# Performance work log

Hardware: AMD Instinct MI355X
Metric: run time of the kernel (lower is better)

Reference implementation:

```python
import jax, jax.numpy as jnp
import numpy as np

B, D_MODEL, D_INNER, N_STATE, K = 128, 2048, 4096, 128, 4


def setup_inputs() -> dict:
    key = jax.random.key(0)
    ks = jax.random.split(key, 10)
    def n(k, shape, s=1.0):
        return jax.random.normal(k, shape, dtype=jnp.float32) * s
    return {
        "x_t": n(ks[0], (B, D_MODEL)),
        "conv_state": n(ks[1], (B, D_INNER, K - 1)),
        "ssm_state": n(ks[2], (B, N_STATE, D_INNER), 0.1),
        "W_in": n(ks[3], (2 * D_INNER, D_MODEL), 0.02),
        "b_in": jnp.zeros((2 * D_INNER,), jnp.float32),
        "conv_weight": n(ks[4], (D_INNER, K), 0.1),
        # A = -exp(A_log) is always negative; sample in (-1, 0) for stability
        "A": -jax.random.uniform(ks[5], (N_STATE, D_INNER), dtype=jnp.float32),
        "B_param": n(ks[6], (N_STATE,), 0.1),
        "C_param": n(ks[7], (N_STATE,), 0.1),
        "D_param": jnp.ones((D_INNER,), jnp.float32),
        "W_out": n(ks[8], (D_MODEL, D_INNER), 0.02),
        "b_out": jnp.zeros((D_MODEL,), jnp.float32),
    }


def reference(x_t, conv_state, ssm_state, W_in, b_in, conv_weight, A,
              B_param, C_param, D_param, W_out, b_out):
    # in_proj, keep first d_inner channels (as in forward())
    x_proj = (x_t @ W_in.T + b_in)[:, :D_INNER]                      # (B, Di)
    # rolling causal conv update: window = [old K-1 samples, new sample]
    window = jnp.concatenate([conv_state, x_proj[:, :, None]], axis=-1)  # (B, Di, K)
    u = jax.nn.silu(jnp.sum(window * conv_weight[None], axis=-1))    # (B, Di)
    new_conv_state = window[:, :, 1:]                                 # (B, Di, K-1)
    # discretized SSM recurrence: h' = exp(A)*h + B u ; y = C.h + D u
    dA = jnp.exp(A)                                                   # (N, Di), in (e^-1, 1)
    new_ssm_state = dA[None] * ssm_state + B_param[None, :, None] * u[:, None, :]  # (B, N, Di)
    y_inner = jnp.einsum('n,bnd->bd', C_param, new_ssm_state) + D_param * u         # (B, Di)
    # out_proj back to d_model
    y_t = y_inner @ W_out.T + b_out                                   # (B, D)
    return (y_t, new_conv_state, new_ssm_state)
```

## Files before the change

### kernel.cpp

```cpp
#include <hip/hip_runtime.h>
#include <hip/hip_bf16.h>

#define DI 4096
#define DM 2048
#define NS 128
#define BB 128

typedef __attribute__((ext_vector_type(8))) short bf16x8;
typedef __attribute__((ext_vector_type(4))) float f32x4;

__device__ __forceinline__ unsigned short f2bf(float f) {
  union { __hip_bfloat16 h; unsigned short u; } c;
  c.h = __float2bfloat16(f);
  return c.u;
}

template<int N, int K, int NSPLIT>
__global__ __launch_bounds__(256) void gemm_bf16(
    const float* __restrict__ Xg, const float* __restrict__ Wg,
    float* __restrict__ part) {
  constexpr int NBLKS = N / 32;
  constexpr int KS = K / NSPLIT;
  constexpr int NSTEPS = KS / 32;
  const int nblk = blockIdx.x % NBLKS;
  const int ks   = blockIdx.x / NBLKS;
  const int kbase = ks * KS;
  const int tid = threadIdx.x;
  const int lane = tid & 63;
  const int wid = tid >> 6;
  const int wr = wid & 1;
  const int wc = wid >> 1;
  const int r16 = lane & 15;
  const int kb = lane >> 4;

  __shared__ __hip_bfloat16 As[128][40];
  __shared__ __hip_bfloat16 Bs[32][40];

  const int arow = tid >> 3;
  const int seg  = tid & 7;

  f32x4 acc[4] = { {0,0,0,0}, {0,0,0,0}, {0,0,0,0}, {0,0,0,0} };

  const float* aG = Xg + (size_t)arow * K + kbase + seg * 4;
  const float* bG = Wg + (size_t)(nblk * 32 + arow) * K + kbase + seg * 4;

  float4 pa0 = *(const float4*)(aG + 0 * 32 * K);
  float4 pa1 = *(const float4*)(aG + 1 * 32 * K);
  float4 pa2 = *(const float4*)(aG + 2 * 32 * K);
  float4 pa3 = *(const float4*)(aG + 3 * 32 * K);
  float4 pb  = *(const float4*)(bG);

  for (int step = 0; step < NSTEPS; ++step) {
    if (step) __syncthreads();
    {
      ushort4 h;
      h.x = f2bf(pa0.x); h.y = f2bf(pa0.y); h.z = f2bf(pa0.z); h.w = f2bf(pa0.w);
      *(ushort4*)&As[arow +  0][seg * 4] = h;
      h.x = f2bf(pa1.x); h.y = f2bf(pa1.y); h.z = f2bf(pa1.z); h.w = f2bf(pa1.w);
      *(ushort4*)&As[arow + 32][seg * 4] = h;
      h.x = f2bf(pa2.x); h.y = f2bf(pa2.y); h.z = f2bf(pa2.z); h.w = f2bf(pa2.w);
      *(ushort4*)&As[arow + 64][seg * 4] = h;
      h.x = f2bf(pa3.x); h.y = f2bf(pa3.y); h.z = f2bf(pa3.z); h.w = f2bf(pa3.w);
      *(ushort4*)&As[arow + 96][seg * 4] = h;
      h.x = f2bf(pb.x);  h.y = f2bf(pb.y);  h.z = f2bf(pb.z);  h.w = f2bf(pb.w);
      *(ushort4*)&Bs[arow][seg * 4] = h;
    }
    if (step + 1 < NSTEPS) {
      const float* aN = aG + (step + 1) * 32;
      pa0 = *(const float4*)(aN + 0 * 32 * K);
      pa1 = *(const float4*)(aN + 1 * 32 * K);
      pa2 = *(const float4*)(aN + 2 * 32 * K);
      pa3 = *(const float4*)(aN + 3 * 32 * K);
      pb  = *(const float4*)(bG + (step + 1) * 32);
    }
    __syncthreads();
    bf16x8 bv = *(const bf16x8*)&Bs[wc * 16 + r16][kb * 8];
#pragma unroll
    for (int m = 0; m < 4; ++m) {
      bf16x8 av = *(const bf16x8*)&As[wr * 64 + m * 16 + r16][kb * 8];
      acc[m] = __builtin_amdgcn_mfma_f32_16x16x32_bf16(av, bv, acc[m], 0, 0, 0);
    }
  }

  const int ncol = nblk * 32 + wc * 16 + r16;
#pragma unroll
  for (int m = 0; m < 4; ++m) {
#pragma unroll
    for (int r = 0; r < 4; ++r) {
      int brow = wr * 64 + m * 16 + kb * 4 + r;
      part[(size_t)(ks * 128 + brow) * N + ncol] = acc[m][r];
    }
  }
}

__global__ __launch_bounds__(256) void combine1(
    const float* __restrict__ part, const float* __restrict__ b_in,
    const float* __restrict__ conv_state, const float* __restrict__ conv_weight,
    float* __restrict__ u_ws, float* __restrict__ ncs) {
  int idx = blockIdx.x * 256 + threadIdx.x;
  int d = idx & (DI - 1);
  float xp = b_in[d];
#pragma unroll
  for (int s = 0; s < 4; ++s) xp += part[(size_t)s * (BB * DI) + idx];
  const float* cs = conv_state + (size_t)idx * 3;
  float4 w4 = *(const float4*)(conv_weight + d * 4);
  float c0 = cs[0], c1 = cs[1], c2 = cs[2];
  float sv = c0 * w4.x + c1 * w4.y + c2 * w4.z + xp * w4.w;
  float uu = sv / (1.f + __expf(-sv));
  u_ws[idx] = uu;
  float* o = ncs + (size_t)idx * 3;
  o[0] = c1; o[1] = c2; o[2] = xp;
}

__global__ __launch_bounds__(256) void ssm_kernel(
    const float* __restrict__ ssm, const float* __restrict__ A,
    const float* __restrict__ Bp, const float* __restrict__ Cp,
    const float* __restrict__ Dp, const float* __restrict__ u,
    float* __restrict__ nss, float* __restrict__ y_in) {
  const int chunk = blockIdx.x >> 7;
  const int b = blockIdx.x & 127;
  const int d0 = chunk * 1024 + threadIdx.x * 4;
  f32x4 u4  = *(const f32x4*)(u + (size_t)b * DI + d0);
  f32x4 dp4 = *(const f32x4*)(Dp + d0);
  float accx = dp4[0]*u4[0], accy = dp4[1]*u4[1];
  float accz = dp4[2]*u4[2], accw = dp4[3]*u4[3];
  const float* sp = ssm + (size_t)b * NS * DI + d0;
  float* op = nss + (size_t)b * NS * DI + d0;
#pragma unroll 4
  for (int i = 0; i < NS; ++i) {
    const int n = (i + b) & (NS - 1);
    f32x4 a4 = *(const f32x4*)(A + (size_t)n * DI + d0);
    f32x4 s4 = __builtin_nontemporal_load((const f32x4*)(sp + (size_t)n * DI));
    float bn = Bp[n], cn = Cp[n];
    f32x4 ns4;
    ns4[0] = __expf(a4[0]) * s4[0] + bn * u4[0];
    ns4[1] = __expf(a4[1]) * s4[1] + bn * u4[1];
    ns4[2] = __expf(a4[2]) * s4[2] + bn * u4[2];
    ns4[3] = __expf(a4[3]) * s4[3] + bn * u4[3];
    __builtin_nontemporal_store(ns4, (f32x4*)(op + (size_t)n * DI));
    accx += cn * ns4[0]; accy += cn * ns4[1];
    accz += cn * ns4[2]; accw += cn * ns4[3];
  }
  f32x4 r; r[0] = accx; r[1] = accy; r[2] = accz; r[3] = accw;
  *(f32x4*)(y_in + (size_t)b * DI + d0) = r;
}

__global__ __launch_bounds__(256) void combine2(
    const float* __restrict__ part, const float* __restrict__ b_out,
    float* __restrict__ y_t) {
  int idx = blockIdx.x * 256 + threadIdx.x;
  int j = idx & (DM - 1);
  float v = b_out[j];
#pragma unroll
  for (int s = 0; s < 8; ++s) v += part[(size_t)s * (BB * DM) + idx];
  y_t[idx] = v;
}

extern "C" void kernel_launch(void* const* d_in, const int* in_sizes, int n_in,
                              void* d_out, int out_size, void* d_ws, size_t ws_size,
                              hipStream_t stream) {
  const float* x_t         = (const float*)d_in[0];
  const float* conv_state  = (const float*)d_in[1];
  const float* ssm_state   = (const float*)d_in[2];
  const float* W_in        = (const float*)d_in[3];
  const float* b_in        = (const float*)d_in[4];
  const float* conv_weight = (const float*)d_in[5];
  const float* A           = (const float*)d_in[6];
  const float* Bp          = (const float*)d_in[7];
  const float* Cp          = (const float*)d_in[8];
  const float* Dp          = (const float*)d_in[9];
  const float* W_out       = (const float*)d_in[10];
  const float* b_out       = (const float*)d_in[11];

  float* y_t = (float*)d_out;
  float* ncs = y_t + (size_t)BB * DM;
  float* nss = ncs + (size_t)BB * DI * 3;

  float* ws = (float*)d_ws;
  const size_t P1 = 4u * BB * DI;
  const size_t P2 = 8u * BB * DM;
  const size_t UV = (size_t)BB * DI;
  float *part1, *part2, *u_ws, *y_in;
  if (ws_size >= (P1 + P2 + 2 * UV) * sizeof(float)) {
    part1 = ws; part2 = part1 + P1; u_ws = part2 + P2; y_in = u_ws + UV;
  } else {
    part1 = nss;
    part2 = ws; u_ws = part2 + P2; y_in = u_ws + UV;
  }

  gemm_bf16<DI, DM, 4><<<dim3(512), dim3(256), 0, stream>>>(x_t, W_in, part1);
  combine1<<<dim3(2048), dim3(256), 0, stream>>>(part1, b_in, conv_state,
                                                 conv_weight, u_ws, ncs);
  ssm_kernel<<<dim3(512), dim3(256), 0, stream>>>(ssm_state, A, Bp, Cp, Dp,
                                                  u_ws, nss, y_in);
  gemm_bf16<DM, DI, 8><<<dim3(512), dim3(256), 0, stream>>>(y_in, W_out, part2);
  combine2<<<dim3(1024), dim3(256), 0, stream>>>(part2, b_out, y_t);
}
```

Measured before the change: 153.4 us.

## Fuse all five stages into one cooperative kernel with grid syncs

Replaces the five separate launches with a single cooperative kernel of 512 blocks that runs the in-projection GEMM, the conv/SiLU combine, the SSM update, the out-projection GEMM and the final reduction as phases separated by grid.sync(). It also precomputes exp(A) once into workspace instead of once per batch row, vectorizes the combine phases, and drops the per-batch rotation of the state loop order. This is meant to remove launch gaps and redundant exp work, at the cost of grid-wide barriers and of relying on all 512 blocks being co-resident. The non-cooperative multi-kernel path is kept as a fallback.

```diff
diff --git a/kernel.cpp b/kernel.cpp
--- a/kernel.cpp
+++ b/kernel.cpp
@@ -1,10 +1,14 @@
 #include <hip/hip_runtime.h>
 #include <hip/hip_bf16.h>
+#include <hip/hip_cooperative_groups.h>
+
+namespace cg = cooperative_groups;
 
 #define DI 4096
 #define DM 2048
 #define NS 128
 #define BB 128
+#define NTHREADS 256
 
 typedef __attribute__((ext_vector_type(8))) short bf16x8;
 typedef __attribute__((ext_vector_type(4))) float f32x4;
@@ -16,25 +20,22 @@
 }
 
 template<int N, int K, int NSPLIT>
-__global__ __launch_bounds__(256) void gemm_bf16(
+__device__ __forceinline__ void gemm_phase(
     const float* __restrict__ Xg, const float* __restrict__ Wg,
-    float* __restrict__ part) {
+    float* part, __hip_bfloat16 (*As)[40], __hip_bfloat16 (*Bs)[40],
+    int bid, int tid) {
   constexpr int NBLKS = N / 32;
   constexpr int KS = K / NSPLIT;
   constexpr int NSTEPS = KS / 32;
-  const int nblk = blockIdx.x % NBLKS;
-  const int ks   = blockIdx.x / NBLKS;
+  const int nblk = bid % NBLKS;
+  const int ks   = bid / NBLKS;
   const int kbase = ks * KS;
-  const int tid = threadIdx.x;
   const int lane = tid & 63;
   const int wid = tid >> 6;
   const int wr = wid & 1;
   const int wc = wid >> 1;
   const int r16 = lane & 15;
   const int kb = lane >> 4;
-
-  __shared__ __hip_bfloat16 As[128][40];
-  __shared__ __hip_bfloat16 Bs[32][40];
 
   const int arow = tid >> 3;
   const int seg  = tid & 7;
@@ -66,12 +67,12 @@
       *(ushort4*)&Bs[arow][seg * 4] = h;
     }
     if (step + 1 < NSTEPS) {
-      const float* aN = aG + (step + 1) * 32;
-      pa0 = *(const float4*)(aN + 0 * 32 * K);
-      pa1 = *(const float4*)(aN + 1 * 32 * K);
-      pa2 = *(const float4*)(aN + 2 * 32 * K);
-      pa3 = *(const float4*)(aN + 3 * 32 * K);
-      pb  = *(const float4*)(bG + (step + 1) * 32);
+      const int o = (step + 1) * 32;
+      pa0 = *(const float4*)(aG + o + 0 * 32 * K);
+      pa1 = *(const float4*)(aG + o + 1 * 32 * K);
+      pa2 = *(const float4*)(aG + o + 2 * 32 * K);
+      pa3 = *(const float4*)(aG + o + 3 * 32 * K);
+      pb  = *(const float4*)(bG + o);
     }
     __syncthreads();
     bf16x8 bv = *(const bf16x8*)&Bs[wc * 16 + r16][kb * 8];
@@ -91,6 +92,121 @@
       part[(size_t)(ks * 128 + brow) * N + ncol] = acc[m][r];
     }
   }
+}
+
+__global__ __launch_bounds__(256, 2) void fused_all(
+    const float* x_t, const float* conv_state, const float* ssm,
+    const float* W_in, const float* b_in, const float* conv_weight,
+    const float* A, const float* Bp, const float* Cp, const float* Dp,
+    const float* W_out, const float* b_out,
+    float* y_t, float* ncs, float* nss,
+    float* part1, float* part2, float* u_ws, float* y_in, float* dAe) {
+  __shared__ __hip_bfloat16 As[128][40];
+  __shared__ __hip_bfloat16 Bs[32][40];
+  const int bid = blockIdx.x;
+  const int tid = threadIdx.x;
+  cg::grid_group grid = cg::this_grid();
+
+  gemm_phase<DI, DM, 4>(x_t, W_in, part1, As, Bs, bid, tid);
+  grid.sync();
+
+  {
+    const int t = bid * NTHREADS + tid;
+    const size_t idx = (size_t)t * 4;
+    const int d0 = (int)(idx & (DI - 1));
+    f32x4 xp = *(const f32x4*)(b_in + d0);
+#pragma unroll
+    for (int s = 0; s < 4; ++s) {
+      f32x4 p = *(const f32x4*)(part1 + (size_t)s * (BB * DI) + idx);
+      xp[0] += p[0]; xp[1] += p[1]; xp[2] += p[2]; xp[3] += p[3];
+    }
+    const float* cs = conv_state + idx * 3;
+    f32x4 cv0 = *(const f32x4*)(cs);
+    f32x4 cv1 = *(const f32x4*)(cs + 4);
+    f32x4 cv2 = *(const f32x4*)(cs + 8);
+    float4 w0 = *(const float4*)(conv_weight + (size_t)(d0 + 0) * 4);
+    float4 w1 = *(const float4*)(conv_weight + (size_t)(d0 + 1) * 4);
+    float4 w2 = *(const float4*)(conv_weight + (size_t)(d0 + 2) * 4);
+    float4 w3 = *(const float4*)(conv_weight + (size_t)(d0 + 3) * 4);
+    float sv0 = cv0[0]*w0.x + cv0[1]*w0.y + cv0[2]*w0.z + xp[0]*w0.w;
+    float sv1 = cv0[3]*w1.x + cv1[0]*w1.y + cv1[1]*w1.z + xp[1]*w1.w;
+    float sv2 = cv1[2]*w2.x + cv1[3]*w2.y + cv2[0]*w2.z + xp[2]*w2.w;
+    float sv3 = cv2[1]*w3.x + cv2[2]*w3.y + cv2[3]*w3.z + xp[3]*w3.w;
+    f32x4 u4;
+    u4[0] = sv0 / (1.f + __expf(-sv0));
+    u4[1] = sv1 / (1.f + __expf(-sv1));
+    u4[2] = sv2 / (1.f + __expf(-sv2));
+    u4[3] = sv3 / (1.f + __expf(-sv3));
+    *(f32x4*)(u_ws + idx) = u4;
+    f32x4 n0, n1, n2;
+    n0[0] = cv0[1]; n0[1] = cv0[2]; n0[2] = xp[0]; n0[3] = cv1[0];
+    n1[0] = cv1[1]; n1[1] = xp[1];  n1[2] = cv1[3]; n1[3] = cv2[0];
+    n2[0] = xp[2];  n2[1] = cv2[2]; n2[2] = cv2[3]; n2[3] = xp[3];
+    float* on = ncs + idx * 3;
+    *(f32x4*)(on)     = n0;
+    *(f32x4*)(on + 4) = n1;
+    *(f32x4*)(on + 8) = n2;
+    f32x4 a4 = *(const f32x4*)(A + idx);
+    f32x4 e4;
+    e4[0] = __expf(a4[0]); e4[1] = __expf(a4[1]);
+    e4[2] = __expf(a4[2]); e4[3] = __expf(a4[3]);
+    *(f32x4*)(dAe + idx) = e4;
+  }
+  grid.sync();
+
+  {
+    const int chunk = bid >> 7;
+    const int b = bid & 127;
+    const int d0 = chunk * 1024 + tid * 4;
+    f32x4 u4  = *(const f32x4*)(u_ws + (size_t)b * DI + d0);
+    f32x4 dp4 = *(const f32x4*)(Dp + d0);
+    float accx = dp4[0]*u4[0], accy = dp4[1]*u4[1];
+    float accz = dp4[2]*u4[2], accw = dp4[3]*u4[3];
+    const float* sp = ssm + (size_t)b * NS * DI + d0;
+    float* op = nss + (size_t)b * NS * DI + d0;
+#pragma unroll 4
+    for (int n = 0; n < NS; ++n) {
+      f32x4 a4 = *(const f32x4*)(dAe + (size_t)n * DI + d0);
+      f32x4 s4 = __builtin_nontemporal_load((const f32x4*)(sp + (size_t)n * DI));
+      float bn = Bp[n], cn = Cp[n];
+      f32x4 ns4;
+      ns4[0] = a4[0] * s4[0] + bn * u4[0];
+      ns4[1] = a4[1] * s4[1] + bn * u4[1];
+      ns4[2] = a4[2] * s4[2] + bn * u4[2];
+      ns4[3] = a4[3] * s4[3] + bn * u4[3];
+      __builtin_nontemporal_store(ns4, (f32x4*)(op + (size_t)n * DI));
+      accx += cn * ns4[0]; accy += cn * ns4[1];
+      accz += cn * ns4[2]; accw += cn * ns4[3];
+    }
+    f32x4 r; r[0] = accx; r[1] = accy; r[2] = accz; r[3] = accw;
+    *(f32x4*)(y_in + (size_t)b * DI + d0) = r;
+  }
+  grid.sync();
+
+  gemm_phase<DM, DI, 8>(y_in, W_out, part2, As, Bs, bid, tid);
+  grid.sync();
+
+  {
+    const int t = bid * NTHREADS + tid;
+    const int idx = t * 2;
+    const int j = idx & (DM - 1);
+    float2 v = *(const float2*)(b_out + j);
+#pragma unroll
+    for (int s = 0; s < 8; ++s) {
+      float2 p = *(const float2*)(part2 + (size_t)s * (BB * DM) + idx);
+      v.x += p.x; v.y += p.y;
+    }
+    *(float2*)(y_t + idx) = v;
+  }
+}
+
+template<int N, int K, int NSPLIT>
+__global__ __launch_bounds__(256) void gemm_bf16(
+    const float* __restrict__ Xg, const float* __restrict__ Wg,
+    float* __restrict__ part) {
+  __shared__ __hip_bfloat16 As[128][40];
+  __shared__ __hip_bfloat16 Bs[32][40];
+  gemm_phase<N, K, NSPLIT>(Xg, Wg, part, As, Bs, blockIdx.x, threadIdx.x);
 }
 
 __global__ __launch_bounds__(256) void combine1(
@@ -127,8 +243,7 @@
   const float* sp = ssm + (size_t)b * NS * DI + d0;
   float* op = nss + (size_t)b * NS * DI + d0;
 #pragma unroll 4
-  for (int i = 0; i < NS; ++i) {
-    const int n = (i + b) & (NS - 1);
+  for (int n = 0; n < NS; ++n) {
     f32x4 a4 = *(const f32x4*)(A + (size_t)n * DI + d0);
     f32x4 s4 = __builtin_nontemporal_load((const f32x4*)(sp + (size_t)n * DI));
     float bn = Bp[n], cn = Cp[n];
@@ -180,19 +295,50 @@
   const size_t P1 = 4u * BB * DI;
   const size_t P2 = 8u * BB * DM;
   const size_t UV = (size_t)BB * DI;
-  float *part1, *part2, *u_ws, *y_in;
-  if (ws_size >= (P1 + P2 + 2 * UV) * sizeof(float)) {
-    part1 = ws; part2 = part1 + P1; u_ws = part2 + P2; y_in = u_ws + UV;
+  const size_t DA = (size_t)NS * DI;
+
+  float *part1, *part2, *u_ws, *y_in, *dAe;
+  bool ws_big = ws_size >= (P1 + P2 + 2 * UV + DA) * sizeof(float);
+  if (ws_big) {
+    part1 = ws; part2 = part1 + P1; u_ws = part2 + P2;
+    y_in = u_ws + UV; dAe = y_in + UV;
   } else {
     part1 = nss;
-    part2 = ws; u_ws = part2 + P2; y_in = u_ws + UV;
-  }
-
-  gemm_bf16<DI, DM, 4><<<dim3(512), dim3(256), 0, stream>>>(x_t, W_in, part1);
-  combine1<<<dim3(2048), dim3(256), 0, stream>>>(part1, b_in, conv_state,
-                                                 conv_weight, u_ws, ncs);
-  ssm_kernel<<<dim3(512), dim3(256), 0, stream>>>(ssm_state, A, Bp, Cp, Dp,
-                                                  u_ws, nss, y_in);
-  gemm_bf16<DM, DI, 8><<<dim3(512), dim3(256), 0, stream>>>(y_in, W_out, part2);
-  combine2<<<dim3(1024), dim3(256), 0, stream>>>(part2, b_out, y_t);
-}
+    part2 = ws; u_ws = part2 + P2; y_in = u_ws + UV; dAe = y_in + UV;
+  }
+
+  bool fused_ok = false;
+  if (ws_size >= (P2 + 2 * UV + DA) * sizeof(float)) {
+    int dev = 0, coop = 0;
+    hipGetDevice(&dev);
+    hipDeviceGetAttribute(&coop, hipDeviceAttributeCooperativeLaunch, dev);
+    if (coop) {
+      void* args[] = {
+        (void*)&x_t, (void*)&conv_state, (void*)&ssm_state,
+        (void*)&W_in, (void*)&b_in, (void*)&conv_weight,
+        (void*)&A, (void*)&Bp, (void*)&Cp, (void*)&Dp,
+        (void*)&W_out, (void*)&b_out,
+        (void*)&y_t, (void*)&ncs, (void*)&nss,
+        (void*)&part1, (void*)&part2, (void*)&u_ws, (void*)&y_in, (void*)&dAe
+      };
+      hipError_t e = hipLaunchCooperativeKernel(
+          (const void*)fused_all, dim3(512), dim3(NTHREADS), args, 0, stream);
+      fused_ok = (e == hipSuccess);
+    }
+  }
+  if (fused_ok) return;
+
+  {
+    float* p1 = nss;
+    float* p2 = ws;
+    float* uw = p2 + P2;
+    float* yi = uw + UV;
+    gemm_bf16<DI, DM, 4><<<dim3(512), dim3(256), 0, stream>>>(x_t, W_in, p1);
+    combine1<<<dim3(2048), dim3(256), 0, stream>>>(p1, b_in, conv_state,
+                                                   conv_weight, uw, ncs);
+    ssm_kernel<<<dim3(512), dim3(256), 0, stream>>>(ssm_state, A, Bp, Cp, Dp,
+                                                    uw, nss, yi);
+    gemm_bf16<DM, DI, 8><<<dim3(512), dim3(256), 0, stream>>>(yi, W_out, p2);
+    combine2<<<dim3(1024), dim3(256), 0, stream>>>(p2, b_out, y_t);
+  }
+}
```

Result: slower. 399.0 us (+160.1%).

## Restructure SSM kernel into contiguous-row halves and fuse partial sums into out-proj GEMM

Applied to the files above, without the earlier changes.

Replaces the 512-block SSM kernel with a 1024-thread-block kernel. Each block covers one batch row's full 4096-wide d range for half of the N states, so every state row is read and written as one contiguous 16KB stretch. The two N-halves write separate partial y buffers, and the out-projection GEMM now sums them while loading its A operand, so no extra reduction pass is needed. Workspace use also shrinks: the in-proj partials go into the nss output buffer and u shares space with part2, which makes the fast path more likely to be taken. The trade-off is fewer, larger blocks for the bandwidth-bound SSM stream and extra loads inside the GEMM.

```diff
diff --git a/kernel.cpp b/kernel.cpp
--- a/kernel.cpp
+++ b/kernel.cpp
@@ -15,10 +15,21 @@
   return c.u;
 }
 
-template<int N, int K, int NSPLIT>
+template<int NSUM>
+__device__ __forceinline__ float4 ldsum(const float* p, size_t str) {
+  float4 a = *(const float4*)p;
+#pragma unroll
+  for (int j = 1; j < NSUM; ++j) {
+    float4 t = *(const float4*)(p + (size_t)j * str);
+    a.x += t.x; a.y += t.y; a.z += t.z; a.w += t.w;
+  }
+  return a;
+}
+
+template<int N, int K, int NSPLIT, int NSUM>
 __global__ __launch_bounds__(256) void gemm_bf16(
-    const float* __restrict__ Xg, const float* __restrict__ Wg,
-    float* __restrict__ part) {
+    const float* __restrict__ Xg, size_t xstr,
+    const float* __restrict__ Wg, float* __restrict__ part) {
   constexpr int NBLKS = N / 32;
   constexpr int KS = K / NSPLIT;
   constexpr int NSTEPS = KS / 32;
@@ -44,10 +55,10 @@
   const float* aG = Xg + (size_t)arow * K + kbase + seg * 4;
   const float* bG = Wg + (size_t)(nblk * 32 + arow) * K + kbase + seg * 4;
 
-  float4 pa0 = *(const float4*)(aG + 0 * 32 * K);
-  float4 pa1 = *(const float4*)(aG + 1 * 32 * K);
-  float4 pa2 = *(const float4*)(aG + 2 * 32 * K);
-  float4 pa3 = *(const float4*)(aG + 3 * 32 * K);
+  float4 pa0 = ldsum<NSUM>(aG + 0 * 32 * K, xstr);
+  float4 pa1 = ldsum<NSUM>(aG + 1 * 32 * K, xstr);
+  float4 pa2 = ldsum<NSUM>(aG + 2 * 32 * K, xstr);
+  float4 pa3 = ldsum<NSUM>(aG + 3 * 32 * K, xstr);
   float4 pb  = *(const float4*)(bG);
 
   for (int step = 0; step < NSTEPS; ++step) {
@@ -66,12 +77,12 @@
       *(ushort4*)&Bs[arow][seg * 4] = h;
     }
     if (step + 1 < NSTEPS) {
-      const float* aN = aG + (step + 1) * 32;
-      pa0 = *(const float4*)(aN + 0 * 32 * K);
-      pa1 = *(const float4*)(aN + 1 * 32 * K);
-      pa2 = *(const float4*)(aN + 2 * 32 * K);
-      pa3 = *(const float4*)(aN + 3 * 32 * K);
-      pb  = *(const float4*)(bG + (step + 1) * 32);
+      const int o = (step + 1) * 32;
+      pa0 = ldsum<NSUM>(aG + o + 0 * 32 * K, xstr);
+      pa1 = ldsum<NSUM>(aG + o + 1 * 32 * K, xstr);
+      pa2 = ldsum<NSUM>(aG + o + 2 * 32 * K, xstr);
+      pa3 = ldsum<NSUM>(aG + o + 3 * 32 * K, xstr);
+      pb  = *(const float4*)(bG + o);
     }
     __syncthreads();
     bf16x8 bv = *(const bf16x8*)&Bs[wc * 16 + r16][kb * 8];
@@ -110,6 +121,45 @@
   u_ws[idx] = uu;
   float* o = ncs + (size_t)idx * 3;
   o[0] = c1; o[1] = c2; o[2] = xp;
+}
+
+__global__ __launch_bounds__(1024) void ssm_contig(
+    const float* __restrict__ ssm, const float* __restrict__ A,
+    const float* __restrict__ Bp, const float* __restrict__ Cp,
+    const float* __restrict__ Dp, const float* __restrict__ u,
+    float* __restrict__ nss, float* __restrict__ yq) {
+  const int b = blockIdx.x & 127;
+  const int q = blockIdx.x >> 7;
+  const int n0 = q * (NS / 2);
+  const int d0 = threadIdx.x * 4;
+  f32x4 u4 = *(const f32x4*)(u + (size_t)b * DI + d0);
+  float accx, accy, accz, accw;
+  if (q == 0) {
+    f32x4 dp4 = *(const f32x4*)(Dp + d0);
+    accx = dp4[0]*u4[0]; accy = dp4[1]*u4[1];
+    accz = dp4[2]*u4[2]; accw = dp4[3]*u4[3];
+  } else {
+    accx = accy = accz = accw = 0.f;
+  }
+  const float* sp = ssm + ((size_t)b * NS + n0) * DI + d0;
+  float* op = nss + ((size_t)b * NS + n0) * DI + d0;
+  const float* ap = A + (size_t)n0 * DI + d0;
+#pragma unroll 4
+  for (int i = 0; i < NS / 2; ++i) {
+    f32x4 a4 = *(const f32x4*)(ap + (size_t)i * DI);
+    f32x4 s4 = __builtin_nontemporal_load((const f32x4*)(sp + (size_t)i * DI));
+    float bn = Bp[n0 + i], cn = Cp[n0 + i];
+    f32x4 ns4;
+    ns4[0] = __expf(a4[0]) * s4[0] + bn * u4[0];
+    ns4[1] = __expf(a4[1]) * s4[1] + bn * u4[1];
+    ns4[2] = __expf(a4[2]) * s4[2] + bn * u4[2];
+    ns4[3] = __expf(a4[3]) * s4[3] + bn * u4[3];
+    __builtin_nontemporal_store(ns4, (f32x4*)(op + (size_t)i * DI));
+    accx += cn * ns4[0]; accy += cn * ns4[1];
+    accz += cn * ns4[2]; accw += cn * ns4[3];
+  }
+  f32x4 r; r[0] = accx; r[1] = accy; r[2] = accz; r[3] = accw;
+  *(f32x4*)(yq + (size_t)q * (BB * DI) + (size_t)b * DI + d0) = r;
 }
 
 __global__ __launch_bounds__(256) void ssm_kernel(
@@ -127,8 +177,7 @@
   const float* sp = ssm + (size_t)b * NS * DI + d0;
   float* op = nss + (size_t)b * NS * DI + d0;
 #pragma unroll 4
-  for (int i = 0; i < NS; ++i) {
-    const int n = (i + b) & (NS - 1);
+  for (int n = 0; n < NS; ++n) {
     f32x4 a4 = *(const f32x4*)(A + (size_t)n * DI + d0);
     f32x4 s4 = __builtin_nontemporal_load((const f32x4*)(sp + (size_t)n * DI));
     float bn = Bp[n], cn = Cp[n];
@@ -145,6 +194,7 @@
   *(f32x4*)(y_in + (size_t)b * DI + d0) = r;
 }
 
+template<int NSPL>
 __global__ __launch_bounds__(256) void combine2(
     const float* __restrict__ part, const float* __restrict__ b_out,
     float* __restrict__ y_t) {
@@ -152,7 +202,7 @@
   int j = idx & (DM - 1);
   float v = b_out[j];
 #pragma unroll
-  for (int s = 0; s < 8; ++s) v += part[(size_t)s * (BB * DM) + idx];
+  for (int s = 0; s < NSPL; ++s) v += part[(size_t)s * (BB * DM) + idx];
   y_t[idx] = v;
 }
 
@@ -177,22 +227,37 @@
   float* nss = ncs + (size_t)BB * DI * 3;
 
   float* ws = (float*)d_ws;
-  const size_t P1 = 4u * BB * DI;
   const size_t P2 = 8u * BB * DM;
   const size_t UV = (size_t)BB * DI;
-  float *part1, *part2, *u_ws, *y_in;
-  if (ws_size >= (P1 + P2 + 2 * UV) * sizeof(float)) {
-    part1 = ws; part2 = part1 + P1; u_ws = part2 + P2; y_in = u_ws + UV;
+
+  if (ws_size >= (P2 + 2 * UV) * sizeof(float)) {
+    float* part1 = nss;
+    float* part2 = ws;
+    float* u_ws  = ws;
+    float* yq    = ws + P2;
+
+    gemm_bf16<DI, DM, 4, 1><<<dim3(512), dim3(256), 0, stream>>>(
+        x_t, 0, W_in, part1);
+    combine1<<<dim3(2048), dim3(256), 0, stream>>>(
+        part1, b_in, conv_state, conv_weight, u_ws, ncs);
+    ssm_contig<<<dim3(256), dim3(1024), 0, stream>>>(
+        ssm_state, A, Bp, Cp, Dp, u_ws, nss, yq);
+    gemm_bf16<DM, DI, 8, 2><<<dim3(512), dim3(256), 0, stream>>>(
+        yq, UV, W_out, part2);
+    combine2<8><<<dim3(1024), dim3(256), 0, stream>>>(part2, b_out, y_t);
   } else {
-    part1 = nss;
-    part2 = ws; u_ws = part2 + P2; y_in = u_ws + UV;
-  }
-
-  gemm_bf16<DI, DM, 4><<<dim3(512), dim3(256), 0, stream>>>(x_t, W_in, part1);
-  combine1<<<dim3(2048), dim3(256), 0, stream>>>(part1, b_in, conv_state,
-                                                 conv_weight, u_ws, ncs);
-  ssm_kernel<<<dim3(512), dim3(256), 0, stream>>>(ssm_state, A, Bp, Cp, Dp,
-                                                  u_ws, nss, y_in);
-  gemm_bf16<DM, DI, 8><<<dim3(512), dim3(256), 0, stream>>>(y_in, W_out, part2);
-  combine2<<<dim3(1024), dim3(256), 0, stream>>>(part2, b_out, y_t);
-}
+    float* p1 = nss;
+    float* p2 = ws;
+    float* uw = p2 + P2;
+    float* yi = uw + UV;
+    gemm_bf16<DI, DM, 4, 1><<<dim3(512), dim3(256), 0, stream>>>(
+        x_t, 0, W_in, p1);
+    combine1<<<dim3(2048), dim3(256), 0, stream>>>(p1, b_in, conv_state,
+                                                   conv_weight, uw, ncs);
+    ssm_kernel<<<dim3(512), dim3(256), 0, stream>>>(ssm_state, A, Bp, Cp, Dp,
+                                                    uw, nss, yi);
+    gemm_bf16<DM, DI, 8, 1><<<dim3(512), dim3(256), 0, stream>>>(
+        yi, 0, W_out, p2);
+    combine2<8><<<dim3(1024), dim3(256), 0, stream>>>(p2, b_out, y_t);
+  }
+}
```

New measurement: 148.0 us. -3.5%, faster.
